# Kernel tuning notes

Hardware: AMD Instinct MI355X
Metric: run time of the kernel (lower is better)

The kernel has to match this reference:

```python
import jax, jax.numpy as jnp
import numpy as np

RAT_AVG = 0.02  # module-level constant threshold on softmax prob of the true class
BETA = 0.8
B, C = 4096, 50257


def setup_inputs() -> dict:
    key = jax.random.key(0)
    k1, k2 = jax.random.split(key)
    y_pred = jax.random.normal(k1, (B, C), dtype=jnp.float32)
    y = jax.random.randint(k2, (B,), 0, C, dtype=jnp.int32)
    return {"y_pred": y_pred, "y": y}


def reference(y_pred, y):
    b, c = y_pred.shape
    # All the target-construction math uses detached logits in the original.
    p = jax.nn.softmax(jax.lax.stop_gradient(y_pred), axis=1)  # [B, C]

    z_max = jnp.argmax(p, axis=1).astype(jnp.int32)            # [B]
    fy = jnp.take_along_axis(p, y[:, None].astype(jnp.int32), axis=1)[:, 0]  # p[i, y[i]]
    s = (fy < RAT_AVG).astype(jnp.int32)                       # [B] noisy-sample mask

    # kthvalue(clas), kthvalue(clas-1), kthvalue(clas-2) == top-3 values/indices
    vals, idxs = jax.lax.top_k(p, 3)                           # [B, 3] descending
    max_9 = vals[:, 1]
    max9_d = idxs[:, 1].astype(jnp.int32)
    max8_d = idxs[:, 2].astype(jnp.int32)

    # Soft target: top-3 probs renormalized, scattered to their class slots.
    w = vals / jnp.sum(vals, axis=1, keepdims=True)            # [B, 3]
    max3_num = jnp.zeros((b, c), dtype=p.dtype).at[
        jnp.arange(b)[:, None], idxs
    ].add(w)                                                   # [B, C] sparse soft target

    sf = s[:, None].astype(p.dtype)                            # [B, 1]
    t_hard = (1.0 - sf) * jax.nn.one_hot(y, c, dtype=p.dtype)
    t_all = jax.lax.stop_gradient(max3_num * sf + t_hard)      # [B, C]

    # SoftCrossEntropy(y_pred, t_all), reduction='average'
    logp = jax.nn.log_softmax(y_pred, axis=1)
    bootstrap = jnp.sum(-logp * t_all) / b

    ones = jnp.ones_like(s)
    return (
        bootstrap,
        s,
        s * z_max + (ones - s) * (-1),
        s * max9_d + (ones - s) * (-1),
        s * max8_d + (ones - s) * (-1),
        jnp.sum(ones - s),
        s.astype(max_9.dtype) * max_9,
    )
```

## Files before the change

kernel.cpp:

```cpp
#include <hip/hip_runtime.h>
#include <math.h>

#define BB 4096
#define CC 50257
#define C4 (CC / 4)
#define RAT_AVG_F 0.02f
#define IMAX 0x7fffffff

#define OFF_S     1
#define OFF_ZMAX  (1 + BB)
#define OFF_M9D   (1 + 2*BB)
#define OFF_M8D   (1 + 3*BB)
#define OFF_CNT   (1 + 4*BB)
#define OFF_MAX9  (2 + 4*BB)

__device__ __forceinline__ void ins3(float x, int j,
                                     float& v0, int& i0,
                                     float& v1, int& i1,
                                     float& v2, int& i2) {
    bool b0 = x > v0, b1 = x > v1, b2 = x > v2;
    float nv2 = fminf(v1, fmaxf(v2, x));
    float nv1 = fminf(v0, fmaxf(v1, x));
    int   ni1 = b0 ? i0 : (b1 ? j : i1);
    int   ni2 = b1 ? i1 : (b2 ? j : i2);
    v0 = fmaxf(v0, x);
    i0 = b0 ? j : i0;
    v1 = nv1; i1 = ni1;
    v2 = nv2; i2 = ni2;
}

__device__ __forceinline__ void merge1(float xv, int jj,
                                       float& v0, int& i0,
                                       float& v1, int& i1,
                                       float& v2, int& i2) {
    bool b0 = (xv > v0) || (xv == v0 && jj < i0);
    bool b1 = (xv > v1) || (xv == v1 && jj < i1);
    bool b2 = (xv > v2) || (xv == v2 && jj < i2);
    float nv1 = b0 ? v0 : (b1 ? xv : v1);
    int   ni1 = b0 ? i0 : (b1 ? jj : i1);
    float nv2 = b1 ? v1 : (b2 ? xv : v2);
    int   ni2 = b1 ? i1 : (b2 ? jj : i2);
    v0 = b0 ? xv : v0; i0 = b0 ? jj : i0;
    v1 = nv1; i1 = ni1;
    v2 = nv2; i2 = ni2;
}

__global__ __launch_bounds__(256) void row_stats_kernel(const float* __restrict__ y_pred,
                                                        const int* __restrict__ y,
                                                        float* __restrict__ out,
                                                        float* __restrict__ boot_ws) {
    const int row = blockIdx.x;
    const int tid = threadIdx.x;
    const float* rp = y_pred + (size_t)row * CC;
    const float4* rp4 = (const float4*)rp;

    float xy = 0.0f;
    if (tid == 0) { int lbl = y[row]; xy = rp[lbl]; }

    float a0 = -INFINITY, a1 = -INFINITY, a2 = -INFINITY;
    int   ai0 = IMAX, ai1 = IMAX, ai2 = IMAX;
    float c0 = -INFINITY, c1 = -INFINITY, c2 = -INFINITY;
    int   ci0 = IMAX, ci1 = IMAX, ci2 = IMAX;
    float sumA = 0.0f, sumB = 0.0f;

    int i = tid;
    for (; i + 256 < C4; i += 512) {
        float4 xa = rp4[i];
        float4 xb = rp4[i + 256];
        int ja = i << 2;
        int jb = ja + 1024;
        sumA += (__expf(xa.x) + __expf(xa.y)) + (__expf(xa.z) + __expf(xa.w));
        sumB += (__expf(xb.x) + __expf(xb.y)) + (__expf(xb.z) + __expf(xb.w));
        ins3(xa.x, ja,     a0, ai0, a1, ai1, a2, ai2);
        ins3(xa.y, ja + 1, a0, ai0, a1, ai1, a2, ai2);
        ins3(xa.z, ja + 2, a0, ai0, a1, ai1, a2, ai2);
        ins3(xa.w, ja + 3, a0, ai0, a1, ai1, a2, ai2);
        ins3(xb.x, jb,     c0, ci0, c1, ci1, c2, ci2);
        ins3(xb.y, jb + 1, c0, ci0, c1, ci1, c2, ci2);
        ins3(xb.z, jb + 2, c0, ci0, c1, ci1, c2, ci2);
        ins3(xb.w, jb + 3, c0, ci0, c1, ci1, c2, ci2);
    }
    for (; i < C4; i += 256) {
        float4 xa = rp4[i];
        int ja = i << 2;
        sumA += (__expf(xa.x) + __expf(xa.y)) + (__expf(xa.z) + __expf(xa.w));
        ins3(xa.x, ja,     a0, ai0, a1, ai1, a2, ai2);
        ins3(xa.y, ja + 1, a0, ai0, a1, ai1, a2, ai2);
        ins3(xa.z, ja + 2, a0, ai0, a1, ai1, a2, ai2);
        ins3(xa.w, ja + 3, a0, ai0, a1, ai1, a2, ai2);
    }
    if (tid == 0) {
        float x = rp[CC - 1];
        sumA += __expf(x);
        ins3(x, CC - 1, a0, ai0, a1, ai1, a2, ai2);
    }

    merge1(c0, ci0, a0, ai0, a1, ai1, a2, ai2);
    merge1(c1, ci1, a0, ai0, a1, ai1, a2, ai2);
    merge1(c2, ci2, a0, ai0, a1, ai1, a2, ai2);
    float sum = sumA + sumB;

    #pragma unroll
    for (int off = 32; off; off >>= 1) {
        float ov0 = __shfl_down(a0, off), ov1 = __shfl_down(a1, off), ov2 = __shfl_down(a2, off);
        int   oi0 = __shfl_down(ai0, off), oi1 = __shfl_down(ai1, off), oi2 = __shfl_down(ai2, off);
        sum += __shfl_down(sum, off);
        merge1(ov0, oi0, a0, ai0, a1, ai1, a2, ai2);
        merge1(ov1, oi1, a0, ai0, a1, ai1, a2, ai2);
        merge1(ov2, oi2, a0, ai0, a1, ai1, a2, ai2);
    }

    __shared__ float sv0[4], sv1[4], sv2[4], ssum[4];
    __shared__ int   si0[4], si1[4], si2[4];
    if ((tid & 63) == 0) {
        int w = tid >> 6;
        sv0[w] = a0; sv1[w] = a1; sv2[w] = a2; ssum[w] = sum;
        si0[w] = ai0; si1[w] = ai1; si2[w] = ai2;
    }
    __syncthreads();

    if (tid == 0) {
        #pragma unroll
        for (int w = 1; w < 4; ++w) {
            sum += ssum[w];
            merge1(sv0[w], si0[w], a0, ai0, a1, ai1, a2, ai2);
            merge1(sv1[w], si1[w], a0, ai0, a1, ai1, a2, ai2);
            merge1(sv2[w], si2[w], a0, ai0, a1, ai1, a2, ai2);
        }
        float S    = sum;
        float logS = __logf(S);
        float fy   = __expf(xy) / S;
        bool  sflg = fy < RAT_AVG_F;

        float e0 = __expf(a0), e1 = __expf(a1), e2 = __expf(a2);
        float boot;
        if (sflg) {
            float inv_w = 1.0f / (e0 + e1 + e2);
            boot = -(e0 * (a0 - logS) + e1 * (a1 - logS) + e2 * (a2 - logS)) * inv_w;
        } else {
            boot = -(xy - logS);
        }
        boot_ws[row]        = boot;
        out[OFF_S + row]    = sflg ? 1.0f : 0.0f;
        out[OFF_ZMAX + row] = sflg ? (float)ai0 : -1.0f;
        out[OFF_M9D + row]  = sflg ? (float)ai1 : -1.0f;
        out[OFF_M8D + row]  = sflg ? (float)ai2 : -1.0f;
        out[OFF_MAX9 + row] = sflg ? (e1 / S) : 0.0f;
    }
}

__global__ __launch_bounds__(256) void final_reduce_kernel(const float* __restrict__ boot_ws,
                                                           float* __restrict__ out) {
    const int tid = threadIdx.x;
    float bsum = 0.0f, csum = 0.0f;
    for (int i = tid; i < BB; i += 256) {
        bsum += boot_ws[i];
        csum += 1.0f - out[OFF_S + i];
    }
    #pragma unroll
    for (int off = 32; off; off >>= 1) {
        bsum += __shfl_down(bsum, off);
        csum += __shfl_down(csum, off);
    }
    __shared__ float sb[4], sc[4];
    if ((tid & 63) == 0) { sb[tid >> 6] = bsum; sc[tid >> 6] = csum; }
    __syncthreads();
    if (tid == 0) {
        float b = 0.0f, c = 0.0f;
        #pragma unroll
        for (int w = 0; w < 4; ++w) { b += sb[w]; c += sc[w]; }
        out[0]       = b / (float)BB;
        out[OFF_CNT] = c;
    }
}

extern "C" void kernel_launch(void* const* d_in, const int* in_sizes, int n_in,
                              void* d_out, int out_size, void* d_ws, size_t ws_size,
                              hipStream_t stream) {
    const float* y_pred = (const float*)d_in[0];
    const int*   y      = (const int*)d_in[1];
    float* out     = (float*)d_out;
    float* boot_ws = (float*)d_ws;

    row_stats_kernel<<<BB, 256, 0, stream>>>(y_pred, y, out, boot_ws);
    final_reduce_kernel<<<1, 256, 0, stream>>>(boot_ws, out);
}
```

Before: 1.043 ms.

## Replace per-element top-3 insertion with chunk-max prefilter in shared memory

The streaming pass now only computes exp sums and writes a per-float4 chunk maximum into shared memory (about 50KB per block). Top-3 selection runs over these chunk maxima, and thread 0 then re-reads the three winning chunks from global memory to find the exact top-3 elements. This cuts the per-element compare/select work in the bandwidth-bound main loop. In exchange it adds a large LDS allocation that may limit occupancy, an extra barrier, and a serial tail on one thread.

```diff
diff --git a/kernel.cpp b/kernel.cpp
--- a/kernel.cpp
+++ b/kernel.cpp
@@ -4,6 +4,7 @@
 #define BB 4096
 #define CC 50257
 #define C4 (CC / 4)
+#define NCHUNK (C4 + 1)
 #define RAT_AVG_F 0.02f
 #define IMAX 0x7fffffff
 
@@ -49,6 +50,11 @@
                                                         const int* __restrict__ y,
                                                         float* __restrict__ out,
                                                         float* __restrict__ boot_ws) {
+    __shared__ float smax[NCHUNK];
+    __shared__ float ssum[4];
+    __shared__ float sv0[4], sv1[4], sv2[4];
+    __shared__ int   si0[4], si1[4], si2[4];
+
     const int row = blockIdx.x;
     const int tid = threadIdx.x;
     const float* rp = y_pred + (size_t)row * CC;
@@ -57,95 +63,100 @@
     float xy = 0.0f;
     if (tid == 0) { int lbl = y[row]; xy = rp[lbl]; }
 
-    float a0 = -INFINITY, a1 = -INFINITY, a2 = -INFINITY;
-    int   ai0 = IMAX, ai1 = IMAX, ai2 = IMAX;
-    float c0 = -INFINITY, c1 = -INFINITY, c2 = -INFINITY;
-    int   ci0 = IMAX, ci1 = IMAX, ci2 = IMAX;
     float sumA = 0.0f, sumB = 0.0f;
-
     int i = tid;
     for (; i + 256 < C4; i += 512) {
         float4 xa = rp4[i];
         float4 xb = rp4[i + 256];
-        int ja = i << 2;
-        int jb = ja + 1024;
         sumA += (__expf(xa.x) + __expf(xa.y)) + (__expf(xa.z) + __expf(xa.w));
         sumB += (__expf(xb.x) + __expf(xb.y)) + (__expf(xb.z) + __expf(xb.w));
-        ins3(xa.x, ja,     a0, ai0, a1, ai1, a2, ai2);
-        ins3(xa.y, ja + 1, a0, ai0, a1, ai1, a2, ai2);
-        ins3(xa.z, ja + 2, a0, ai0, a1, ai1, a2, ai2);
-        ins3(xa.w, ja + 3, a0, ai0, a1, ai1, a2, ai2);
-        ins3(xb.x, jb,     c0, ci0, c1, ci1, c2, ci2);
-        ins3(xb.y, jb + 1, c0, ci0, c1, ci1, c2, ci2);
-        ins3(xb.z, jb + 2, c0, ci0, c1, ci1, c2, ci2);
-        ins3(xb.w, jb + 3, c0, ci0, c1, ci1, c2, ci2);
+        smax[i]       = fmaxf(fmaxf(xa.x, xa.y), fmaxf(xa.z, xa.w));
+        smax[i + 256] = fmaxf(fmaxf(xb.x, xb.y), fmaxf(xb.z, xb.w));
     }
     for (; i < C4; i += 256) {
         float4 xa = rp4[i];
-        int ja = i << 2;
         sumA += (__expf(xa.x) + __expf(xa.y)) + (__expf(xa.z) + __expf(xa.w));
-        ins3(xa.x, ja,     a0, ai0, a1, ai1, a2, ai2);
-        ins3(xa.y, ja + 1, a0, ai0, a1, ai1, a2, ai2);
-        ins3(xa.z, ja + 2, a0, ai0, a1, ai1, a2, ai2);
-        ins3(xa.w, ja + 3, a0, ai0, a1, ai1, a2, ai2);
+        smax[i] = fmaxf(fmaxf(xa.x, xa.y), fmaxf(xa.z, xa.w));
     }
     if (tid == 0) {
         float x = rp[CC - 1];
         sumA += __expf(x);
-        ins3(x, CC - 1, a0, ai0, a1, ai1, a2, ai2);
+        smax[C4] = x;
     }
-
-    merge1(c0, ci0, a0, ai0, a1, ai1, a2, ai2);
-    merge1(c1, ci1, a0, ai0, a1, ai1, a2, ai2);
-    merge1(c2, ci2, a0, ai0, a1, ai1, a2, ai2);
     float sum = sumA + sumB;
 
     #pragma unroll
+    for (int off = 32; off; off >>= 1) sum += __shfl_down(sum, off);
+    if ((tid & 63) == 0) ssum[tid >> 6] = sum;
+
+    __syncthreads();
+
+    float v0 = -INFINITY, v1 = -INFINITY, v2 = -INFINITY;
+    int   c0 = IMAX, c1 = IMAX, c2 = IMAX;
+    for (int k = tid; k < NCHUNK; k += 256)
+        ins3(smax[k], k, v0, c0, v1, c1, v2, c2);
+
+    #pragma unroll
     for (int off = 32; off; off >>= 1) {
-        float ov0 = __shfl_down(a0, off), ov1 = __shfl_down(a1, off), ov2 = __shfl_down(a2, off);
-        int   oi0 = __shfl_down(ai0, off), oi1 = __shfl_down(ai1, off), oi2 = __shfl_down(ai2, off);
-        sum += __shfl_down(sum, off);
-        merge1(ov0, oi0, a0, ai0, a1, ai1, a2, ai2);
-        merge1(ov1, oi1, a0, ai0, a1, ai1, a2, ai2);
-        merge1(ov2, oi2, a0, ai0, a1, ai1, a2, ai2);
+        float ov0 = __shfl_down(v0, off), ov1 = __shfl_down(v1, off), ov2 = __shfl_down(v2, off);
+        int   oc0 = __shfl_down(c0, off), oc1 = __shfl_down(c1, off), oc2 = __shfl_down(c2, off);
+        merge1(ov0, oc0, v0, c0, v1, c1, v2, c2);
+        merge1(ov1, oc1, v0, c0, v1, c1, v2, c2);
+        merge1(ov2, oc2, v0, c0, v1, c1, v2, c2);
     }
-
-    __shared__ float sv0[4], sv1[4], sv2[4], ssum[4];
-    __shared__ int   si0[4], si1[4], si2[4];
     if ((tid & 63) == 0) {
         int w = tid >> 6;
-        sv0[w] = a0; sv1[w] = a1; sv2[w] = a2; ssum[w] = sum;
-        si0[w] = ai0; si1[w] = ai1; si2[w] = ai2;
+        sv0[w] = v0; sv1[w] = v1; sv2[w] = v2;
+        si0[w] = c0; si1[w] = c1; si2[w] = c2;
     }
     __syncthreads();
 
     if (tid == 0) {
+        float S = sum;
         #pragma unroll
         for (int w = 1; w < 4; ++w) {
-            sum += ssum[w];
-            merge1(sv0[w], si0[w], a0, ai0, a1, ai1, a2, ai2);
-            merge1(sv1[w], si1[w], a0, ai0, a1, ai1, a2, ai2);
-            merge1(sv2[w], si2[w], a0, ai0, a1, ai1, a2, ai2);
+            S += ssum[w];
+            merge1(sv0[w], si0[w], v0, c0, v1, c1, v2, c2);
+            merge1(sv1[w], si1[w], v0, c0, v1, c1, v2, c2);
+            merge1(sv2[w], si2[w], v0, c0, v1, c1, v2, c2);
         }
-        float S    = sum;
+
+        float e0v = -INFINITY, e1v = -INFINITY, e2v = -INFINITY;
+        int   e0i = IMAX, e1i = IMAX, e2i = IMAX;
+        int chs0 = c0, chs1 = c1, chs2 = c2;
+        #pragma unroll
+        for (int t = 0; t < 3; ++t) {
+            int c = (t == 0) ? chs0 : (t == 1) ? chs1 : chs2;
+            if (c < C4) {
+                float4 q = rp4[c];
+                int b = c << 2;
+                merge1(q.x, b,     e0v, e0i, e1v, e1i, e2v, e2i);
+                merge1(q.y, b + 1, e0v, e0i, e1v, e1i, e2v, e2i);
+                merge1(q.z, b + 2, e0v, e0i, e1v, e1i, e2v, e2i);
+                merge1(q.w, b + 3, e0v, e0i, e1v, e1i, e2v, e2i);
+            } else {
+                merge1(rp[CC - 1], CC - 1, e0v, e0i, e1v, e1i, e2v, e2i);
+            }
+        }
+
         float logS = __logf(S);
         float fy   = __expf(xy) / S;
         bool  sflg = fy < RAT_AVG_F;
 
-        float e0 = __expf(a0), e1 = __expf(a1), e2 = __expf(a2);
+        float x0 = __expf(e0v), x1 = __expf(e1v), x2 = __expf(e2v);
         float boot;
         if (sflg) {
-            float inv_w = 1.0f / (e0 + e1 + e2);
-            boot = -(e0 * (a0 - logS) + e1 * (a1 - logS) + e2 * (a2 - logS)) * inv_w;
+            float inv_w = 1.0f / (x0 + x1 + x2);
+            boot = -(x0 * (e0v - logS) + x1 * (e1v - logS) + x2 * (e2v - logS)) * inv_w;
         } else {
             boot = -(xy - logS);
         }
         boot_ws[row]        = boot;
         out[OFF_S + row]    = sflg ? 1.0f : 0.0f;
-        out[OFF_ZMAX + row] = sflg ? (float)ai0 : -1.0f;
-        out[OFF_M9D + row]  = sflg ? (float)ai1 : -1.0f;
-        out[OFF_M8D + row]  = sflg ? (float)ai2 : -1.0f;
-        out[OFF_MAX9 + row] = sflg ? (e1 / S) : 0.0f;
+        out[OFF_ZMAX + row] = sflg ? (float)e0i : -1.0f;
+        out[OFF_M9D + row]  = sflg ? (float)e1i : -1.0f;
+        out[OFF_M8D + row]  = sflg ? (float)e2i : -1.0f;
+        out[OFF_MAX9 + row] = sflg ? (x1 / S) : 0.0f;
     }
 }
 
```

Measured after the change: 1.070 ms. 2.6% more time.
